# Performance work log

Hardware: AMD Instinct MI355X
Metric: run time of the kernel (lower is better)

Reference implementation:

```python
import jax, jax.numpy as jnp
import numpy as np

DIM = 128
NUM_HEADS = 8
HEAD_DIM = DIM // NUM_HEADS
N_NODES = 50000
N_EDGES = 800000


def setup_inputs() -> dict:
    key = jax.random.key(0)
    ks = jax.random.split(key, 10)
    scale = 1.0 / np.sqrt(DIM)
    x = jax.random.normal(ks[0], (N_NODES, DIM), dtype=jnp.float32)
    edge_index = jax.random.randint(ks[1], (2, N_EDGES), 0, N_NODES, dtype=jnp.int64)
    Wq = jax.random.normal(ks[2], (DIM, DIM), dtype=jnp.float32) * scale
    bq = jnp.zeros((DIM,), dtype=jnp.float32)
    Wk = jax.random.normal(ks[3], (DIM, DIM), dtype=jnp.float32) * scale
    bk = jnp.zeros((DIM,), dtype=jnp.float32)
    Wv = jax.random.normal(ks[4], (DIM, DIM), dtype=jnp.float32) * scale
    bv = jnp.zeros((DIM,), dtype=jnp.float32)
    Wo = jax.random.normal(ks[5], (DIM, DIM), dtype=jnp.float32) * scale
    bo = jnp.zeros((DIM,), dtype=jnp.float32)
    return {"x": x, "edge_index": edge_index, "Wq": Wq, "bq": bq,
            "Wk": Wk, "bk": bk, "Wv": Wv, "bv": bv, "Wo": Wo, "bo": bo}


def reference(x, edge_index, Wq, bq, Wk, bk, Wv, bv, Wo, bo):
    n = x.shape[0]
    tgt = edge_index[0]  # softmax group / scatter destination
    src = edge_index[1]  # gather source
    # projections: torch nn.Linear -> x @ W.T + b
    q = (x @ Wq.T + bq).reshape(n, NUM_HEADS, HEAD_DIM)
    k = (x @ Wk.T + bk).reshape(n, NUM_HEADS, HEAD_DIM)
    v = (x @ Wv.T + bv).reshape(n, NUM_HEADS, HEAD_DIM)
    # edge-wise attention scores: [E, H]
    scores = jnp.einsum('ehd,ehd->eh', q[src], k[tgt]) / np.sqrt(HEAD_DIM).astype(np.float32)
    # segment softmax over edges grouped by target node
    m = jax.ops.segment_max(scores, tgt, num_segments=n)          # [N, H]
    m = jax.lax.stop_gradient(m)
    p = jnp.exp(scores - m[tgt])                                   # [E, H]
    s = jax.ops.segment_sum(p, tgt, num_segments=n)               # [N, H]
    probs = p / s[tgt]
    # weighted scatter-add of source values
    weighted = v[src] * probs[..., None]                           # [E, H, D]
    agg = jax.ops.segment_sum(weighted, tgt, num_segments=n)      # [N, H, D]
    out = agg.reshape(n, DIM) @ Wo.T + bo
    # dropout is identity in eval mode
    return out
```

## Files before the change

### kernel.cpp

```cpp
#include <hip/hip_runtime.h>
#include <math.h>

#define NN 50000
#define NE 800000
#define DIM 128
#define NH 8
#define HD 16
#define NTILE 3125
#define TPB 782
#define LROW 136
#define QVROW 256
#define SCAN_B 196

typedef short v8s __attribute__((ext_vector_type(8)));
typedef float v4f __attribute__((ext_vector_type(4)));

__device__ __forceinline__ unsigned short f2b(float f) {
    unsigned u = __float_as_uint(f);
    u = (u + 0x7fffu + ((u >> 16) & 1u)) >> 16;
    return (unsigned short)u;
}
__device__ __forceinline__ float blo(unsigned w) { return __uint_as_float(w << 16); }
__device__ __forceinline__ float bhi(unsigned w) { return __uint_as_float(w & 0xffff0000u); }

template<int PAT>
__device__ __forceinline__ float swz(float x) {
    return __int_as_float(__builtin_amdgcn_ds_swizzle(__float_as_int(x), PAT));
}

#define NW4 (4 * DIM * DIM / 4)
#define NC4 ((NN + 3) / 4)
__global__ __launch_bounds__(256) void convert_kernel(
    const float* __restrict__ Wq, const float* __restrict__ Wk,
    const float* __restrict__ Wv, const float* __restrict__ Wo,
    unsigned short* __restrict__ Wb, int* __restrict__ cnt)
{
    int i = blockIdx.x * 256 + threadIdx.x;
    if (i < NW4) {
        int mat = i >> 12;
        int off = i & 4095;
        const float* Wsrc = (mat == 0) ? Wq : (mat == 1) ? Wk : (mat == 2) ? Wv : Wo;
        float4 f = ((const float4*)Wsrc)[off];
        uint2 o;
        o.x = (unsigned)f2b(f.x) | ((unsigned)f2b(f.y) << 16);
        o.y = (unsigned)f2b(f.z) | ((unsigned)f2b(f.w) << 16);
        ((uint2*)(Wb + (size_t)mat * DIM * DIM))[off] = o;
    } else if (i < NW4 + NC4) {
        ((int4*)cnt)[i - NW4] = make_int4(0, 0, 0, 0);
    }
}

__global__ __launch_bounds__(256) void qkv_mfma_kernel(
    const float* __restrict__ x, const unsigned short* __restrict__ Wb,
    const float* __restrict__ bq, const float* __restrict__ bk, const float* __restrict__ bv,
    unsigned short* __restrict__ qvb, unsigned short* __restrict__ kb,
    const int* __restrict__ tgt, int* __restrict__ cnt)
{
    __shared__ unsigned short Wl[DIM * LROW];
    const int mat = blockIdx.x / TPB;
    const int tg  = blockIdx.x % TPB;
    const int tid = threadIdx.x;
    const int lane = tid & 63;
    const int warp = tid >> 6;
    const int m = lane & 15;
    const int quad = lane >> 4;

    const int gsize = 3 * TPB * 256;
    for (int e = blockIdx.x * 256 + tid; e < NE; e += gsize)
        atomicAdd(cnt + tgt[e], 1);

    const unsigned short* Wg = Wb + (size_t)mat * DIM * DIM;
#pragma unroll
    for (int it = 0; it < 8; ++it) {
        int chunk = it * 256 + tid;
        int row = chunk >> 4, c8 = chunk & 15;
        *(uint4*)(Wl + row * LROW + c8 * 8) = ((const uint4*)Wg)[chunk];
    }
    __syncthreads();

    const int rt = tg * 4 + warp;
    if (rt >= NTILE) return;
    const int r0 = rt * 16;

    const float* bias_p = (mat == 0) ? bq : (mat == 1) ? bk : bv;

    v8s a[4];
#pragma unroll
    for (int kt = 0; kt < 4; ++kt) {
        const float4* xr = (const float4*)(x + (size_t)(r0 + m) * DIM + kt * 32 + quad * 8);
        float4 f0 = xr[0], f1 = xr[1];
        v8s t;
        t[0] = (short)f2b(f0.x); t[1] = (short)f2b(f0.y);
        t[2] = (short)f2b(f0.z); t[3] = (short)f2b(f0.w);
        t[4] = (short)f2b(f1.x); t[5] = (short)f2b(f1.y);
        t[6] = (short)f2b(f1.z); t[7] = (short)f2b(f1.w);
        a[kt] = t;
    }

    const int i0 = (lane & 1) ? 2 : 0;

#pragma unroll
    for (int nt = 0; nt < 8; ++nt) {
        v4f c = {0.f, 0.f, 0.f, 0.f};
#pragma unroll
        for (int kt = 0; kt < 4; ++kt) {
            v8s b = *(const v8s*)(Wl + (nt * 16 + m) * LROW + kt * 32 + quad * 8);
            c = __builtin_amdgcn_mfma_f32_16x16x32_bf16(a[kt], b, c, 0, 0, 0);
        }
        int col = nt * 16 + m;
        float bias = bias_p[col];
        unsigned w0 = 0, w1 = 0;
#pragma unroll
        for (int i = 0; i < 4; ++i) {
            unsigned own  = (unsigned)f2b(c[i] + bias);
            unsigned part = (unsigned)__builtin_amdgcn_ds_swizzle((int)own, 0x041F) & 0xffffu;
            unsigned w = (lane & 1) ? (part | (own << 16)) : (own | (part << 16));
            if (i == i0)     w0 = w;
            if (i == i0 + 1) w1 = w;
        }
        int colb = nt * 16 + (m & ~1);
        int rowa = r0 + quad * 4 + i0;
        if (mat == 1) {
            *(unsigned*)(kb + (size_t)rowa * DIM + colb)       = w0;
            *(unsigned*)(kb + (size_t)(rowa + 1) * DIM + colb) = w1;
        } else {
            int pos = colb * 2 + ((mat == 2) ? 2 : 0);
            *(unsigned*)(qvb + (size_t)rowa * QVROW + pos)       = w0;
            *(unsigned*)(qvb + (size_t)(rowa + 1) * QVROW + pos) = w1;
        }
    }
}

__global__ __launch_bounds__(256) void scan1_kernel(
    const int* __restrict__ cnt, int* __restrict__ off, int* __restrict__ bsum)
{
    __shared__ int ws4[4];
    const int tid = threadIdx.x, lane = tid & 63, wid = tid >> 6;
    int i = blockIdx.x * 256 + tid;
    int v0 = (i < NN) ? cnt[i] : 0;
    int incl = v0;
#pragma unroll
    for (int d = 1; d < 64; d <<= 1) {
        int t = __shfl_up(incl, d);
        if (lane >= d) incl += t;
    }
    if (lane == 63) ws4[wid] = incl;
    __syncthreads();
    int wexcl = 0;
#pragma unroll
    for (int t = 0; t < 3; ++t) if (t < wid) wexcl += ws4[t];
    if (i < NN) off[i] = wexcl + incl - v0;
    if (tid == 255) bsum[blockIdx.x] = wexcl + incl;
}

__global__ __launch_bounds__(256) void scan23_kernel(
    const int* __restrict__ bsum, int* __restrict__ off, int* __restrict__ cursor)
{
    __shared__ int ws4[4];
    __shared__ int base_s, total_s;
    const int tid = threadIdx.x, lane = tid & 63, wid = tid >> 6;
    int v0 = (tid < SCAN_B) ? bsum[tid] : 0;
    int incl = v0;
#pragma unroll
    for (int d = 1; d < 64; d <<= 1) {
        int t = __shfl_up(incl, d);
        if (lane >= d) incl += t;
    }
    if (lane == 63) ws4[wid] = incl;
    __syncthreads();
    int wexcl = 0;
#pragma unroll
    for (int t = 0; t < 3; ++t) if (t < wid) wexcl += ws4[t];
    int excl = wexcl + incl - v0;
    if (tid == blockIdx.x) base_s = excl;
    if (tid == SCAN_B - 1) total_s = excl + v0;
    __syncthreads();
    int i = blockIdx.x * 256 + tid;
    if (i < NN) {
        int t = off[i] + base_s;
        off[i] = t;
        cursor[i] = t;
    }
    if (blockIdx.x == SCAN_B - 1 && tid == 0) off[NN] = total_s;
}

__global__ __launch_bounds__(256) void fill_kernel(
    const int* __restrict__ tgt, const int* __restrict__ src,
    int* __restrict__ cursor, int* __restrict__ edge_src)
{
    int e = blockIdx.x * 256 + threadIdx.x;
    if (e >= NE) return;
    int t = tgt[e];
    int pos = atomicAdd(cursor + t, 1);
    edge_src[pos] = src[e];
}

__global__ __launch_bounds__(256) void attn_kernel(
    const int* __restrict__ off, const int* __restrict__ edge_src,
    const unsigned short* __restrict__ qvb, const unsigned short* __restrict__ kb,
    unsigned short* __restrict__ aggb)
{
    const int tid = threadIdx.x;
    const int lane = tid & 63;
    const int node = blockIdx.x * 4 + (tid >> 6);
    if (node >= NN) return;

    const int base = __builtin_amdgcn_readfirstlane(off[node]);
    const int deg  = __builtin_amdgcn_readfirstlane(off[node + 1]) - base;

    unsigned kw = *(const unsigned*)(kb + (size_t)node * DIM + 2 * lane);
    const float klo = blo(kw), khi = bhi(kw);
    const int j = lane & 7;

    float ax = 0.f, ay = 0.f, ss = 0.f;

    for (int c0 = 0; c0 < deg; c0 += 64) {
        const int nchunk = min(deg - c0, 64);
        int srcv = edge_src[base + c0 + min(lane, nchunk - 1)];
        for (int b = 0; b < nchunk; b += 8) {
            const int nb = min(nchunk - b, 8);
            uint2 qv[8];
#pragma unroll
            for (int i = 0; i < 8; ++i) {
                int si = __builtin_amdgcn_readlane(srcv, min(b + i, nchunk - 1));
                qv[i] = ((const uint2*)(qvb + (size_t)si * QVROW))[lane];
            }
            float part[8];
#pragma unroll
            for (int i = 0; i < 8; ++i)
                part[i] = blo(qv[i].x) * klo + bhi(qv[i].x) * khi;
            float r1[4];
#pragma unroll
            for (int t = 0; t < 4; ++t) {
                float keep = (j & 1) ? part[2 * t + 1] : part[2 * t];
                float send = (j & 1) ? part[2 * t]     : part[2 * t + 1];
                r1[t] = keep + swz<0x041F>(send);
            }
            float r2[2];
#pragma unroll
            for (int u = 0; u < 2; ++u) {
                float keep = (j & 2) ? r1[2 * u + 1] : r1[2 * u];
                float send = (j & 2) ? r1[2 * u]     : r1[2 * u + 1];
                r2[u] = keep + swz<0x081F>(send);
            }
            float keep = (j & 4) ? r2[1] : r2[0];
            float send = (j & 4) ? r2[0] : r2[1];
            float tot = keep + swz<0x101F>(send);
            float p = (j < nb) ? __expf(tot * 0.25f) : 0.f;
            ss += p;
#define ACC(i) { float pi = swz<((i) << 5) | 0x18>(p); unsigned vv = qv[i].y; \
                 ax += pi * blo(vv); ay += pi * bhi(vv); }
            ACC(0) ACC(1) ACC(2) ACC(3) ACC(4) ACC(5) ACC(6) ACC(7)
#undef ACC
        }
    }
    ss += swz<0x041F>(ss);
    ss += swz<0x081F>(ss);
    ss += swz<0x101F>(ss);

    unsigned* ap = (unsigned*)(aggb + (size_t)node * DIM + 2 * lane);
    if (deg == 0) {
        *ap = 0u;
    } else {
        float inv = 1.f / ss;
        *ap = (unsigned)f2b(ax * inv) | ((unsigned)f2b(ay * inv) << 16);
    }
}

__global__ __launch_bounds__(256) void outproj_mfma_kernel(
    const unsigned short* __restrict__ aggb, const unsigned short* __restrict__ Wob,
    const float* __restrict__ bo, float* __restrict__ out)
{
    __shared__ unsigned short Wl[DIM * LROW];
    const int tid = threadIdx.x;
    const int lane = tid & 63;
    const int warp = tid >> 6;
    const int m = lane & 15;
    const int quad = lane >> 4;

#pragma unroll
    for (int it = 0; it < 8; ++it) {
        int chunk = it * 256 + tid;
        int row = chunk >> 4, c8 = chunk & 15;
        *(uint4*)(Wl + row * LROW + c8 * 8) = ((const uint4*)Wob)[chunk];
    }
    __syncthreads();

    const int rt = blockIdx.x * 4 + warp;
    if (rt >= NTILE) return;
    const int r0 = rt * 16;

    v8s a[4];
#pragma unroll
    for (int kt = 0; kt < 4; ++kt)
        a[kt] = *(const v8s*)(aggb + (size_t)(r0 + m) * DIM + kt * 32 + quad * 8);

#pragma unroll
    for (int nt = 0; nt < 8; ++nt) {
        v4f c = {0.f, 0.f, 0.f, 0.f};
#pragma unroll
        for (int kt = 0; kt < 4; ++kt) {
            v8s b = *(const v8s*)(Wl + (nt * 16 + m) * LROW + kt * 32 + quad * 8);
            c = __builtin_amdgcn_mfma_f32_16x16x32_bf16(a[kt], b, c, 0, 0, 0);
        }
        int col = nt * 16 + m;
        float bias = bo[col];
#pragma unroll
        for (int i = 0; i < 4; ++i) {
            int row = r0 + quad * 4 + i;
            out[(size_t)row * DIM + col] = c[i] + bias;
        }
    }
}

extern "C" void kernel_launch(void* const* d_in, const int* in_sizes, int n_in,
                              void* d_out, int out_size, void* d_ws, size_t ws_size,
                              hipStream_t stream) {
    const float* x  = (const float*)d_in[0];
    const int*   ei = (const int*)d_in[1];
    const float* Wq = (const float*)d_in[2];
    const float* bq = (const float*)d_in[3];
    const float* Wk = (const float*)d_in[4];
    const float* bk = (const float*)d_in[5];
    const float* Wv = (const float*)d_in[6];
    const float* bv = (const float*)d_in[7];
    const float* Wo = (const float*)d_in[8];
    const float* bo = (const float*)d_in[9];

    const int* tgt = ei;
    const int* src = ei + NE;

    char* ws = (char*)d_ws;
    const size_t SZ_QV = (size_t)NN * QVROW * 2;
    const size_t SZ_BF = (size_t)NN * DIM * 2;

    unsigned short* qvb  = (unsigned short*)(ws);
    unsigned short* kb   = (unsigned short*)(ws + SZ_QV);
    unsigned short* aggb = (unsigned short*)(ws + SZ_QV + SZ_BF);
    unsigned short* Wb   = (unsigned short*)(ws + SZ_QV + 2 * SZ_BF);

    char* wi = ws + SZ_QV + 2 * SZ_BF + (size_t)4 * DIM * DIM * 2;
    int* cnt      = (int*)(wi);
    int* off      = (int*)(wi + (size_t)NN * 4);
    int* cursor   = (int*)(wi + (size_t)(2 * NN + 1) * 4);
    int* edge_src = (int*)(wi + (size_t)(3 * NN + 1) * 4);
    int* bsum     = (int*)(wi + (size_t)(3 * NN + 1) * 4 + (size_t)NE * 4);

    const int conv_blocks = (NW4 + NC4 + 255) / 256;
    const int edge_blocks = (NE + 255) / 256;

    convert_kernel<<<conv_blocks, 256, 0, stream>>>(Wq, Wk, Wv, Wo, Wb, cnt);
    qkv_mfma_kernel<<<3 * TPB, 256, 0, stream>>>(x, Wb, bq, bk, bv, qvb, kb, tgt, cnt);
    scan1_kernel<<<SCAN_B, 256, 0, stream>>>(cnt, off, bsum);
    scan23_kernel<<<SCAN_B, 256, 0, stream>>>(bsum, off, cursor);
    fill_kernel<<<edge_blocks, 256, 0, stream>>>(tgt, src, cursor, edge_src);
    attn_kernel<<<(NN + 3) / 4, 256, 0, stream>>>(off, edge_src, qvb, kb, aggb);
    outproj_mfma_kernel<<<TPB, 256, 0, stream>>>(
        aggb, Wb + (size_t)3 * DIM * DIM, bo, (float*)d_out);
}
```

Baseline: 248.4 us.

## Split interleaved QV buffer and remap attention lanes to edge-by-head

Stores Q and V in separate row-major bf16 buffers instead of one interleaved buffer. The attention kernel now has each lane handle one edge and one head: it loads 16 q and 16 v values with vector loads, computes the dot product locally and needs no cross-lane swizzle reduction per edge batch. Per-lane partial outputs are reduced across the 8 edge lanes once, at the end. This cuts per-edge shuffle traffic and readlane serialisation, at the cost of more registers (16 accumulators plus 16 k values) and less coalesced, per-lane scattered 32-byte gathers.

```diff
diff --git a/kernel.cpp b/kernel.cpp
--- a/kernel.cpp
+++ b/kernel.cpp
@@ -9,7 +9,6 @@
 #define NTILE 3125
 #define TPB 782
 #define LROW 136
-#define QVROW 256
 #define SCAN_B 196
 
 typedef short v8s __attribute__((ext_vector_type(8)));
@@ -53,7 +52,8 @@
 __global__ __launch_bounds__(256) void qkv_mfma_kernel(
     const float* __restrict__ x, const unsigned short* __restrict__ Wb,
     const float* __restrict__ bq, const float* __restrict__ bk, const float* __restrict__ bv,
-    unsigned short* __restrict__ qvb, unsigned short* __restrict__ kb,
+    unsigned short* __restrict__ qb, unsigned short* __restrict__ kb,
+    unsigned short* __restrict__ vb,
     const int* __restrict__ tgt, int* __restrict__ cnt)
 {
     __shared__ unsigned short Wl[DIM * LROW];
@@ -83,6 +83,7 @@
     const int r0 = rt * 16;
 
     const float* bias_p = (mat == 0) ? bq : (mat == 1) ? bk : bv;
+    unsigned short* dst = (mat == 0) ? qb : (mat == 1) ? kb : vb;
 
     v8s a[4];
 #pragma unroll
@@ -120,14 +121,8 @@
         }
         int colb = nt * 16 + (m & ~1);
         int rowa = r0 + quad * 4 + i0;
-        if (mat == 1) {
-            *(unsigned*)(kb + (size_t)rowa * DIM + colb)       = w0;
-            *(unsigned*)(kb + (size_t)(rowa + 1) * DIM + colb) = w1;
-        } else {
-            int pos = colb * 2 + ((mat == 2) ? 2 : 0);
-            *(unsigned*)(qvb + (size_t)rowa * QVROW + pos)       = w0;
-            *(unsigned*)(qvb + (size_t)(rowa + 1) * QVROW + pos) = w1;
-        }
+        *(unsigned*)(dst + (size_t)rowa * DIM + colb)       = w0;
+        *(unsigned*)(dst + (size_t)(rowa + 1) * DIM + colb) = w1;
     }
 }
 
@@ -197,8 +192,8 @@
 
 __global__ __launch_bounds__(256) void attn_kernel(
     const int* __restrict__ off, const int* __restrict__ edge_src,
-    const unsigned short* __restrict__ qvb, const unsigned short* __restrict__ kb,
-    unsigned short* __restrict__ aggb)
+    const unsigned short* __restrict__ qbuf, const unsigned short* __restrict__ vbuf,
+    const unsigned short* __restrict__ kbuf, unsigned short* __restrict__ aggb)
 {
     const int tid = threadIdx.x;
     const int lane = tid & 63;
@@ -208,51 +203,78 @@
     const int base = __builtin_amdgcn_readfirstlane(off[node]);
     const int deg  = __builtin_amdgcn_readfirstlane(off[node + 1]) - base;
 
-    unsigned kw = *(const unsigned*)(kb + (size_t)node * DIM + 2 * lane);
-    const float klo = blo(kw), khi = bhi(kw);
-    const int j = lane & 7;
-
-    float ax = 0.f, ay = 0.f, ss = 0.f;
+    const int e = lane & 7;
+    const int h = lane >> 3;
+    const unsigned hoff = (unsigned)h * HD;
+
+    float kf[16];
+    {
+        uint4 k0 = *(const uint4*)(kbuf + (size_t)node * DIM + hoff);
+        uint4 k1 = *(const uint4*)(kbuf + (size_t)node * DIM + hoff + 8);
+        unsigned kw[8] = {k0.x, k0.y, k0.z, k0.w, k1.x, k1.y, k1.z, k1.w};
+#pragma unroll
+        for (int i = 0; i < 8; ++i) { kf[2*i] = blo(kw[i]); kf[2*i+1] = bhi(kw[i]); }
+    }
+
+    float acc[16];
+#pragma unroll
+    for (int i = 0; i < 16; ++i) acc[i] = 0.f;
+    float ss = 0.f;
 
     for (int c0 = 0; c0 < deg; c0 += 64) {
         const int nchunk = min(deg - c0, 64);
-        int srcv = edge_src[base + c0 + min(lane, nchunk - 1)];
+        int srcv = edge_src[base + min(c0 + lane, deg - 1)];
         for (int b = 0; b < nchunk; b += 8) {
-            const int nb = min(nchunk - b, 8);
-            uint2 qv[8];
-#pragma unroll
-            for (int i = 0; i < 8; ++i) {
-                int si = __builtin_amdgcn_readlane(srcv, min(b + i, nchunk - 1));
-                qv[i] = ((const uint2*)(qvb + (size_t)si * QVROW))[lane];
-            }
-            float part[8];
-#pragma unroll
-            for (int i = 0; i < 8; ++i)
-                part[i] = blo(qv[i].x) * klo + bhi(qv[i].x) * khi;
-            float r1[4];
-#pragma unroll
-            for (int t = 0; t < 4; ++t) {
-                float keep = (j & 1) ? part[2 * t + 1] : part[2 * t];
-                float send = (j & 1) ? part[2 * t]     : part[2 * t + 1];
-                r1[t] = keep + swz<0x041F>(send);
-            }
-            float r2[2];
-#pragma unroll
-            for (int u = 0; u < 2; ++u) {
-                float keep = (j & 2) ? r1[2 * u + 1] : r1[2 * u];
-                float send = (j & 2) ? r1[2 * u]     : r1[2 * u + 1];
-                r2[u] = keep + swz<0x081F>(send);
-            }
-            float keep = (j & 4) ? r2[1] : r2[0];
-            float send = (j & 4) ? r2[0] : r2[1];
-            float tot = keep + swz<0x101F>(send);
-            float p = (j < nb) ? __expf(tot * 0.25f) : 0.f;
+            const int nb = nchunk - b;
+            int sp = __shfl(srcv, b + e);
+            unsigned qoff = ((unsigned)sp << 7) + hoff;
+            uint4 qa = *(const uint4*)(qbuf + qoff);
+            uint4 qc = *(const uint4*)(qbuf + qoff + 8);
+            uint4 va = *(const uint4*)(vbuf + qoff);
+            uint4 vc = *(const uint4*)(vbuf + qoff + 8);
+            float t0 = 0.f, t1 = 0.f;
+            t0 += blo(qa.x) * kf[0];   t0 += bhi(qa.x) * kf[1];
+            t0 += blo(qa.y) * kf[2];   t0 += bhi(qa.y) * kf[3];
+            t0 += blo(qa.z) * kf[4];   t0 += bhi(qa.z) * kf[5];
+            t0 += blo(qa.w) * kf[6];   t0 += bhi(qa.w) * kf[7];
+            t1 += blo(qc.x) * kf[8];   t1 += bhi(qc.x) * kf[9];
+            t1 += blo(qc.y) * kf[10];  t1 += bhi(qc.y) * kf[11];
+            t1 += blo(qc.z) * kf[12];  t1 += bhi(qc.z) * kf[13];
+            t1 += blo(qc.w) * kf[14];  t1 += bhi(qc.w) * kf[15];
+            float p = __expf((t0 + t1) * 0.25f);
+            if (e >= nb) p = 0.f;
             ss += p;
-#define ACC(i) { float pi = swz<((i) << 5) | 0x18>(p); unsigned vv = qv[i].y; \
-                 ax += pi * blo(vv); ay += pi * bhi(vv); }
-            ACC(0) ACC(1) ACC(2) ACC(3) ACC(4) ACC(5) ACC(6) ACC(7)
-#undef ACC
-        }
+            acc[0]  += p * blo(va.x);  acc[1]  += p * bhi(va.x);
+            acc[2]  += p * blo(va.y);  acc[3]  += p * bhi(va.y);
+            acc[4]  += p * blo(va.z);  acc[5]  += p * bhi(va.z);
+            acc[6]  += p * blo(va.w);  acc[7]  += p * bhi(va.w);
+            acc[8]  += p * blo(vc.x);  acc[9]  += p * bhi(vc.x);
+            acc[10] += p * blo(vc.y);  acc[11] += p * bhi(vc.y);
+            acc[12] += p * blo(vc.z);  acc[13] += p * bhi(vc.z);
+            acc[14] += p * blo(vc.w);  acc[15] += p * bhi(vc.w);
+        }
+    }
+
+    float r8[8];
+#pragma unroll
+    for (int t = 0; t < 8; ++t) {
+        float keep = (e & 4) ? acc[8 + t] : acc[t];
+        float send = (e & 4) ? acc[t]     : acc[8 + t];
+        r8[t] = keep + swz<0x101F>(send);
+    }
+    float r4[4];
+#pragma unroll
+    for (int u = 0; u < 4; ++u) {
+        float keep = (e & 2) ? r8[4 + u] : r8[u];
+        float send = (e & 2) ? r8[u]     : r8[4 + u];
+        r4[u] = keep + swz<0x081F>(send);
+    }
+    float r2[2];
+#pragma unroll
+    for (int w2 = 0; w2 < 2; ++w2) {
+        float keep = (e & 1) ? r4[2 + w2] : r4[w2];
+        float send = (e & 1) ? r4[w2]     : r4[2 + w2];
+        r2[w2] = keep + swz<0x041F>(send);
     }
     ss += swz<0x041F>(ss);
     ss += swz<0x081F>(ss);
@@ -263,7 +285,7 @@
         *ap = 0u;
     } else {
         float inv = 1.f / ss;
-        *ap = (unsigned)f2b(ax * inv) | ((unsigned)f2b(ay * inv) << 16);
+        *ap = (unsigned)f2b(r2[0] * inv) | ((unsigned)f2b(r2[1] * inv) << 16);
     }
 }
 
@@ -331,15 +353,15 @@
     const int* src = ei + NE;
 
     char* ws = (char*)d_ws;
-    const size_t SZ_QV = (size_t)NN * QVROW * 2;
     const size_t SZ_BF = (size_t)NN * DIM * 2;
 
-    unsigned short* qvb  = (unsigned short*)(ws);
-    unsigned short* kb   = (unsigned short*)(ws + SZ_QV);
-    unsigned short* aggb = (unsigned short*)(ws + SZ_QV + SZ_BF);
-    unsigned short* Wb   = (unsigned short*)(ws + SZ_QV + 2 * SZ_BF);
-
-    char* wi = ws + SZ_QV + 2 * SZ_BF + (size_t)4 * DIM * DIM * 2;
+    unsigned short* qb   = (unsigned short*)(ws);
+    unsigned short* kb   = (unsigned short*)(ws + SZ_BF);
+    unsigned short* vb   = (unsigned short*)(ws + 2 * SZ_BF);
+    unsigned short* aggb = (unsigned short*)(ws + 3 * SZ_BF);
+    unsigned short* Wb   = (unsigned short*)(ws + 4 * SZ_BF);
+
+    char* wi = ws + 4 * SZ_BF + (size_t)4 * DIM * DIM * 2;
     int* cnt      = (int*)(wi);
     int* off      = (int*)(wi + (size_t)NN * 4);
     int* cursor   = (int*)(wi + (size_t)(2 * NN + 1) * 4);
@@ -350,11 +372,11 @@
     const int edge_blocks = (NE + 255) / 256;
 
     convert_kernel<<<conv_blocks, 256, 0, stream>>>(Wq, Wk, Wv, Wo, Wb, cnt);
-    qkv_mfma_kernel<<<3 * TPB, 256, 0, stream>>>(x, Wb, bq, bk, bv, qvb, kb, tgt, cnt);
+    qkv_mfma_kernel<<<3 * TPB, 256, 0, stream>>>(x, Wb, bq, bk, bv, qb, kb, vb, tgt, cnt);
     scan1_kernel<<<SCAN_B, 256, 0, stream>>>(cnt, off, bsum);
     scan23_kernel<<<SCAN_B, 256, 0, stream>>>(bsum, off, cursor);
     fill_kernel<<<edge_blocks, 256, 0, stream>>>(tgt, src, cursor, edge_src);
-    attn_kernel<<<(NN + 3) / 4, 256, 0, stream>>>(off, edge_src, qvb, kb, aggb);
+    attn_kernel<<<(NN + 3) / 4, 256, 0, stream>>>(off, edge_src, qb, vb, kb, aggb);
     outproj_mfma_kernel<<<TPB, 256, 0, stream>>>(
         aggb, Wb + (size_t)3 * DIM * DIM, bo, (float*)d_out);
 }
```

New measurement: 251.4 us. No clear change (+1.2%).

## Double-buffer source row gathers in attention kernel to overlap loads with compute

Applied to the files above, without the earlier changes.

Restructures the per-node edge loop so the next group of eight gathered q/v rows is loaded into a second register buffer while the current group's scores, softmax weights and weighted sums are computed. It also adds an occupancy hint to the launch bounds and simplifies index clamping by relying on the per-chunk srcv clamp. The aim is to hide gather latency on the random row accesses, at the cost of higher register pressure from the doubled buffers.

```diff
diff --git a/kernel.cpp b/kernel.cpp
--- a/kernel.cpp
+++ b/kernel.cpp
@@ -195,7 +195,7 @@
     edge_src[pos] = src[e];
 }
 
-__global__ __launch_bounds__(256) void attn_kernel(
+__global__ __launch_bounds__(256, 8) void attn_kernel(
     const int* __restrict__ off, const int* __restrict__ edge_src,
     const unsigned short* __restrict__ qvb, const unsigned short* __restrict__ kb,
     unsigned short* __restrict__ aggb)
@@ -214,46 +214,59 @@
 
     float ax = 0.f, ay = 0.f, ss = 0.f;
 
+    uint2 qvA[8], qvB[8];
+
+#define G1(S, BB, I) { \
+        int si = __builtin_amdgcn_readlane(srcv, (BB) * 8 + (I)); \
+        qv##S[I] = ((const uint2*)(qvb + ((size_t)(unsigned)si << 8)))[lane]; }
+#define GATHER(S, BB) { \
+        G1(S, BB, 0) G1(S, BB, 1) G1(S, BB, 2) G1(S, BB, 3) \
+        G1(S, BB, 4) G1(S, BB, 5) G1(S, BB, 6) G1(S, BB, 7) }
+
+#define ACC1(S, I) { float pi = swz<((I) << 5) | 0x18>(p); \
+        unsigned vv = qv##S[I].y; ax += pi * blo(vv); ay += pi * bhi(vv); }
+
+#define COMPUTE(S, BB) { \
+        const int nbu = nchunk - (BB) * 8; \
+        float part0 = blo(qv##S[0].x) * klo + bhi(qv##S[0].x) * khi; \
+        float part1 = blo(qv##S[1].x) * klo + bhi(qv##S[1].x) * khi; \
+        float part2 = blo(qv##S[2].x) * klo + bhi(qv##S[2].x) * khi; \
+        float part3 = blo(qv##S[3].x) * klo + bhi(qv##S[3].x) * khi; \
+        float part4 = blo(qv##S[4].x) * klo + bhi(qv##S[4].x) * khi; \
+        float part5 = blo(qv##S[5].x) * klo + bhi(qv##S[5].x) * khi; \
+        float part6 = blo(qv##S[6].x) * klo + bhi(qv##S[6].x) * khi; \
+        float part7 = blo(qv##S[7].x) * klo + bhi(qv##S[7].x) * khi; \
+        float r10 = ((j & 1) ? part1 : part0) + swz<0x041F>((j & 1) ? part0 : part1); \
+        float r11 = ((j & 1) ? part3 : part2) + swz<0x041F>((j & 1) ? part2 : part3); \
+        float r12 = ((j & 1) ? part5 : part4) + swz<0x041F>((j & 1) ? part4 : part5); \
+        float r13 = ((j & 1) ? part7 : part6) + swz<0x041F>((j & 1) ? part6 : part7); \
+        float r20 = ((j & 2) ? r11 : r10) + swz<0x081F>((j & 2) ? r10 : r11); \
+        float r21 = ((j & 2) ? r13 : r12) + swz<0x081F>((j & 2) ? r12 : r13); \
+        float tot = ((j & 4) ? r21 : r20) + swz<0x101F>((j & 4) ? r20 : r21); \
+        float p = (j < nbu) ? __expf(tot * 0.25f) : 0.f; \
+        ss += p; \
+        ACC1(S, 0) ACC1(S, 1) ACC1(S, 2) ACC1(S, 3) \
+        ACC1(S, 4) ACC1(S, 5) ACC1(S, 6) ACC1(S, 7) }
+
     for (int c0 = 0; c0 < deg; c0 += 64) {
         const int nchunk = min(deg - c0, 64);
-        int srcv = edge_src[base + c0 + min(lane, nchunk - 1)];
-        for (int b = 0; b < nchunk; b += 8) {
-            const int nb = min(nchunk - b, 8);
-            uint2 qv[8];
-#pragma unroll
-            for (int i = 0; i < 8; ++i) {
-                int si = __builtin_amdgcn_readlane(srcv, min(b + i, nchunk - 1));
-                qv[i] = ((const uint2*)(qvb + (size_t)si * QVROW))[lane];
-            }
-            float part[8];
-#pragma unroll
-            for (int i = 0; i < 8; ++i)
-                part[i] = blo(qv[i].x) * klo + bhi(qv[i].x) * khi;
-            float r1[4];
-#pragma unroll
-            for (int t = 0; t < 4; ++t) {
-                float keep = (j & 1) ? part[2 * t + 1] : part[2 * t];
-                float send = (j & 1) ? part[2 * t]     : part[2 * t + 1];
-                r1[t] = keep + swz<0x041F>(send);
-            }
-            float r2[2];
-#pragma unroll
-            for (int u = 0; u < 2; ++u) {
-                float keep = (j & 2) ? r1[2 * u + 1] : r1[2 * u];
-                float send = (j & 2) ? r1[2 * u]     : r1[2 * u + 1];
-                r2[u] = keep + swz<0x081F>(send);
-            }
-            float keep = (j & 4) ? r2[1] : r2[0];
-            float send = (j & 4) ? r2[0] : r2[1];
-            float tot = keep + swz<0x101F>(send);
-            float p = (j < nb) ? __expf(tot * 0.25f) : 0.f;
-            ss += p;
-#define ACC(i) { float pi = swz<((i) << 5) | 0x18>(p); unsigned vv = qv[i].y; \
-                 ax += pi * blo(vv); ay += pi * bhi(vv); }
-            ACC(0) ACC(1) ACC(2) ACC(3) ACC(4) ACC(5) ACC(6) ACC(7)
-#undef ACC
-        }
-    }
+        int srcv = edge_src[base + min(c0 + lane, deg - 1)];
+        const int nbt = (nchunk + 7) >> 3;
+        GATHER(A, 0);
+        int bb = 0;
+        for (; bb + 2 <= nbt; bb += 2) {
+            GATHER(B, bb + 1);
+            COMPUTE(A, bb);
+            if (bb + 2 < nbt) GATHER(A, bb + 2);
+            COMPUTE(B, bb + 1);
+        }
+        if (bb < nbt) COMPUTE(A, bb);
+    }
+#undef G1
+#undef GATHER
+#undef ACC1
+#undef COMPUTE
+
     ss += swz<0x041F>(ss);
     ss += swz<0x081F>(ss);
     ss += swz<0x101F>(ss);
```

After: 266.3 us. 1.07x slower.
